# Optimization experiments

Hardware: AMD Instinct MI355X
Metric: run time of the kernel (lower is better)

## Reference

```python
import math
import jax, jax.numpy as jnp
import numpy as np

B, S, D = 2, 2048, 3584
H, KVH, HD = 28, 4, 128
ROPE_THETA = 1000000.0

def setup_inputs() -> dict:
    key = jax.random.key(0)
    k1, k2, k3, k4, k5 = jax.random.split(key, 5)
    s = 0.02
    return {
        'hidden_states': jax.random.normal(k1, (B, S, D), jnp.float32),
        'Wq': jax.random.normal(k2, (D, H * HD), jnp.float32) * s,
        'Wk': jax.random.normal(k3, (D, KVH * HD), jnp.float32) * s,
        'Wv': jax.random.normal(k4, (D, KVH * HD), jnp.float32) * s,
        'Wo': jax.random.normal(k5, (H * HD, D), jnp.float32) * s,
    }

def _rotate_half(x):
    x1, x2 = x[..., :x.shape[-1] // 2], x[..., x.shape[-1] // 2:]
    return jnp.concatenate((-x2, x1), axis=-1)

def _rope_tables(seq_len, dim, base):
    inv_freq = 1.0 / base ** (jnp.arange(0, dim, 2, dtype=jnp.float32) / dim)
    t = jnp.arange(seq_len, dtype=jnp.float32)
    freqs = jnp.outer(t, inv_freq)  # [S, dim/2]
    emb = jnp.concatenate((freqs, freqs), axis=-1)  # [S, dim]
    return jnp.cos(emb), jnp.sin(emb)

def reference(hidden_states, Wq, Wk, Wv, Wo):
    b, s, _ = hidden_states.shape
    q = (hidden_states @ Wq).reshape(b, s, H, HD)
    k = (hidden_states @ Wk).reshape(b, s, KVH, HD)
    v = (hidden_states @ Wv).reshape(b, s, KVH, HD)

    cos, sin = _rope_tables(s, HD, ROPE_THETA)
    cos = cos.astype(q.dtype)[None, :, None, :]  # [1,S,1,HD]
    sin = sin.astype(q.dtype)[None, :, None, :]
    q = q * cos + _rotate_half(q) * sin
    k = k * cos + _rotate_half(k) * sin

    groups = H // KVH  # 7
    k = jnp.repeat(k, groups, axis=2)
    v = jnp.repeat(v, groups, axis=2)

    q = jnp.transpose(q, (0, 2, 1, 3))  # [B,H,S,HD]
    k = jnp.transpose(k, (0, 2, 1, 3))
    v = jnp.transpose(v, (0, 2, 1, 3))

    scale = 1.0 / math.sqrt(HD)
    scores = jnp.einsum('bhqd,bhkd->bhqk', q, k) * scale
    causal = jnp.tril(jnp.ones((s, s), dtype=bool))[None, None]
    scores = scores + jnp.where(causal, 0.0, -1e9).astype(scores.dtype)
    attn = jax.nn.softmax(scores, axis=-1)
    out = jnp.einsum('bhqk,bhkd->bhqd', attn, v)
    out = jnp.transpose(out, (0, 2, 1, 3)).reshape(b, s, H * HD)
    return out @ Wo
```

## Files before the change

kernel.cpp:

```cpp
#include <hip/hip_runtime.h>
#include <hip/hip_bf16.h>
#include <cstdint>

typedef __attribute__((ext_vector_type(8))) __bf16 bf16x8;
typedef __attribute__((ext_vector_type(4))) float f32x4;
typedef unsigned short u16;

#define B_    2
#define S_    2048
#define D_    3584
#define H_    28
#define KVH_  4
#define HD_   128
#define GQA_  7
#define QKVN  4608
#define QK2SCALE 0.12751744416014806f

#define WAITV(N) asm volatile("s_waitcnt vmcnt(" #N ")" ::: "memory")
#define WAITL(N) asm volatile("s_waitcnt lgkmcnt(" #N ")" ::: "memory")

__device__ __forceinline__ u16 f2bf(float f){
  union { float f; uint32_t u; } v; v.f = f;
  uint32_t u = v.u + 0x7fffu + ((v.u >> 16) & 1u);
  return (u16)(u >> 16);
}
__device__ __forceinline__ float bf2f(u16 h){
  union { uint32_t u; float f; } v; v.u = ((uint32_t)h) << 16; return v.f;
}
__device__ __forceinline__ float exp2a(float x){
  float r; asm("v_exp_f32 %0, %1" : "=v"(r) : "v"(x)); return r;
}
__device__ __forceinline__ uint32_t cvtpk(float lo, float hi){
  uint32_t r; asm("v_cvt_pk_bf16_f32 %0, %1, %2" : "=v"(r) : "v"(lo), "v"(hi)); return r;
}

typedef void __attribute__((address_space(1))) as1void;
typedef void __attribute__((address_space(3))) as3void;
__device__ __forceinline__ void gload16(const void* g, void* l){
  __builtin_amdgcn_global_load_lds((as1void*)g, (as3void*)l, 16, 0, 0);
}

__global__ __launch_bounds__(256) void convx_kernel(const float* __restrict__ in, u16* __restrict__ outp, int n4){
  int i = blockIdx.x*256 + threadIdx.x;
  if (i < n4){
    float4 v = ((const float4*)in)[i];
    ushort4 o; o.x=f2bf(v.x); o.y=f2bf(v.y); o.z=f2bf(v.z); o.w=f2bf(v.w);
    ((ushort4*)outp)[i] = o;
  }
}

__global__ __launch_bounds__(256) void tconv_kernel(const float* __restrict__ in, u16* __restrict__ outp, int R, int C){
  __shared__ float t[32][33];
  int r = threadIdx.x >> 5, c = threadIdx.x & 31;
  int r0 = blockIdx.y*32, c0 = blockIdx.x*32;
  #pragma unroll
  for (int i=0;i<4;i++) t[r+8*i][c] = in[(size_t)(r0 + r + 8*i)*C + c0 + c];
  __syncthreads();
  #pragma unroll
  for (int i=0;i<4;i++) outp[(size_t)(c0 + r + 8*i)*R + r0 + c] = f2bf(t[c][r+8*i]);
}

__global__ __launch_bounds__(256) void tbf16_kernel(const u16* __restrict__ in, u16* __restrict__ outp, int R, int C, int instride){
  const u16* inb = in + (size_t)blockIdx.z*R*instride;
  u16* outb = outp + (size_t)blockIdx.z*R*C;
  __shared__ u16 t[32][33];
  int r = threadIdx.x >> 5, c = threadIdx.x & 31;
  int r0 = blockIdx.y*32, c0 = blockIdx.x*32;
  #pragma unroll
  for (int i=0;i<4;i++) t[r+8*i][c] = inb[(size_t)(r0+r+8*i)*instride + c0+c];
  __syncthreads();
  #pragma unroll
  for (int i=0;i<4;i++) outb[(size_t)(c0+r+8*i)*R + r0+c] = t[c][r+8*i];
}

__global__ __launch_bounds__(256) void ropetab_kernel(float* __restrict__ cost, float* __restrict__ sint){
  int i = blockIdx.x*256 + threadIdx.x;
  int s = i >> 6, d = i & 63;
  float inv = powf(1.0e6f, -(float)d * (1.0f/64.0f));
  float a = (float)s * inv;
  cost[i] = cosf(a); sint[i] = sinf(a);
}

__global__ __launch_bounds__(256) void rope_kernel(u16* __restrict__ x, const float* __restrict__ cost,
                                                   const float* __restrict__ sint){
  int i = blockIdx.x*256 + threadIdx.x;
  int d = i & 63;
  int h = (i >> 6) & 31;
  int bs = i >> 11;
  int s = bs & (S_-1);
  float sc = (h < H_) ? QK2SCALE : 1.0f;
  size_t base = (size_t)bs*QKVN + (size_t)h*128 + d;
  float x0 = bf2f(x[base]), x1 = bf2f(x[base+64]);
  float cv = cost[s*64+d], sv = sint[s*64+d];
  x[base]    = f2bf((x0*cv - x1*sv)*sc);
  x[base+64] = f2bf((x1*cv + x0*sv)*sc);
}

__global__ __launch_bounds__(256) void gemm128_kernel(const u16* __restrict__ A, const u16* __restrict__ Bt,
                                                      u16* __restrict__ C, int M, int N, int K, int ldc, int coloff){
  __shared__ u16 As[128*32];
  __shared__ u16 Bs[128*32];
  const int tid = threadIdx.x;
  const int l = tid & 63, lg = l >> 4, lm = l & 15;
  const int w = tid >> 6, wr = w >> 1, wc = w & 1;
  const int m0 = blockIdx.y * 128, n0 = blockIdx.x * 128;

  f32x4 acc[4][4];
  #pragma unroll
  for (int m=0;m<4;++m)
    #pragma unroll
    for (int n=0;n<4;++n) acc[m][n] = (f32x4){0.f,0.f,0.f,0.f};

  const int nkt = K >> 5;
  for (int kt = 0; kt < nkt; ++kt){
    __syncthreads();
    const int kb = kt*32;
    #pragma unroll
    for (int j = 0; j < 2; ++j){
      int g = j*256 + tid;
      int row = g >> 2, wi = g & 3;
      int ksrc = kb + ((wi ^ (row & 3)) << 3);
      gload16(A  + (size_t)(m0+row)*K + ksrc, (char*)As + j*4096 + (tid & 192)*16);
      gload16(Bt + (size_t)(n0+row)*K + ksrc, (char*)Bs + j*4096 + (tid & 192)*16);
    }
    __syncthreads();
    bf16x8 af[4], bfr[4];
    #pragma unroll
    for (int m = 0; m < 4; ++m){
      int r = wr*64 + m*16 + lm;
      af[m] = *(const bf16x8*)((const char*)As + r*64 + (lg ^ (r & 3))*16);
    }
    #pragma unroll
    for (int n = 0; n < 4; ++n){
      int r = wc*64 + n*16 + lm;
      bfr[n] = *(const bf16x8*)((const char*)Bs + r*64 + (lg ^ (r & 3))*16);
    }
    #pragma unroll
    for (int m = 0; m < 4; ++m)
      #pragma unroll
      for (int n = 0; n < 4; ++n)
        acc[m][n] = __builtin_amdgcn_mfma_f32_16x16x32_bf16(af[m], bfr[n], acc[m][n], 0,0,0);
  }
  #pragma unroll
  for (int m=0;m<4;++m)
    #pragma unroll
    for (int n=0;n<4;++n)
      #pragma unroll
      for (int r=0;r<4;++r){
        int row = m0 + wr*64 + m*16 + lg*4 + r;
        int col = coloff + n0 + wc*64 + n*16 + lm;
        C[(size_t)row*ldc + col] = f2bf(acc[m][n][r]);
      }
}

template<bool OUTF32>
__global__ __launch_bounds__(512) void gemm256_kernel(const u16* __restrict__ A, const u16* __restrict__ Bt,
                                                      void* __restrict__ Cv, int M, int N, int K, int nbx,
                                                      int ldc, int coloff){
  extern __shared__ char lds[];
  const int tid = threadIdx.x;
  const int l = tid & 63, lg = l >> 4, lm = l & 15;
  const int w = tid >> 6, wr = w >> 2, wc = w & 3;
  const int srow = tid >> 3, swi = tid & 7;

  const int nwg = (int)gridDim.x;
  const int q8 = nwg >> 3, r8 = nwg & 7;
  const int xcd = blockIdx.x & 7, pos = blockIdx.x >> 3;
  const int wg = (xcd < r8 ? xcd*(q8+1) : r8*(q8+1) + (xcd - r8)*q8) + pos;
  const int m0 = (wg / nbx) * 256, n0 = (wg % nbx) * 256;

  f32x4 acc[8][4];
  #pragma unroll
  for (int m=0;m<8;++m)
    #pragma unroll
    for (int n=0;n<4;++n) acc[m][n] = (f32x4){0.f,0.f,0.f,0.f};
  bf16x8 aF[8][2], bF[4][2];

  auto stage = [&](int T, int ht){
    const u16* p = (ht < 2) ? (A + (size_t)(m0 + (ht << 7))*K)
                            : (Bt + (size_t)(n0 + ((ht - 2) << 7))*K);
    char* d = lds + ((size_t)(T & 1) << 16) + (ht << 14) + ((tid & 448) << 4);
    #pragma unroll
    for (int j = 0; j < 2; ++j){
      int r = (j << 6) + srow;
      gload16(p + (size_t)r*K + (size_t)T*64 + ((swi ^ (r & 7)) << 3), d + (j << 13));
    }
  };
  auto ldA = [&](int c, int mh){
    const char* base = lds + (c << 16) + (wr << 14);
    #pragma unroll
    for (int m = 0; m < 4; ++m){
      int r = ((mh*4 + m) << 4) + lm;
      #pragma unroll
      for (int kk = 0; kk < 2; ++kk)
        aF[mh*4+m][kk] = *(const bf16x8*)(base + r*128 + (((kk*4 + lg) ^ (r & 7)) << 4));
    }
  };
  auto ldB = [&](int c, int nh){
    #pragma unroll
    for (int n = 0; n < 2; ++n){
      int rb = wc*64 + ((nh*2 + n) << 4) + lm;
      const char* base = lds + (c << 16) + 32768 + ((rb >> 7) << 14);
      int ri = rb & 127;
      #pragma unroll
      for (int kk = 0; kk < 2; ++kk)
        bF[nh*2+n][kk] = *(const bf16x8*)(base + ri*128 + (((kk*4 + lg) ^ (ri & 7)) << 4));
    }
  };
  auto mmaQ = [&](int mh, int nh){
    __builtin_amdgcn_s_setprio(1);
    #pragma unroll
    for (int m = 0; m < 4; ++m)
      #pragma unroll
      for (int n = 0; n < 2; ++n)
        #pragma unroll
        for (int kk = 0; kk < 2; ++kk)
          acc[mh*4+m][nh*2+n] = __builtin_amdgcn_mfma_f32_16x16x32_bf16(
              aF[mh*4+m][kk], bF[nh*2+n][kk], acc[mh*4+m][nh*2+n], 0,0,0);
    __builtin_amdgcn_s_setprio(0);
  };

  const int nkt = K >> 6;
  stage(0,0); stage(0,1); stage(0,2); stage(0,3);
  stage(1,2); stage(1,0); stage(1,1);
  WAITV(6);
  __builtin_amdgcn_s_barrier();

  for (int t = 0; t < nkt; ++t){
    const int c = t & 1;
    ldA(c,0); ldB(c,0); ldB(c,1);
    if (t + 1 < nkt) stage(t+1, 3);
    WAITL(4);
    __builtin_amdgcn_s_barrier();
    mmaQ(0,0);
    WAITL(0);
    __builtin_amdgcn_s_barrier();
    ldA(c,1);
    if (t + 2 < nkt) stage(t+2, 2);
    __builtin_amdgcn_s_barrier();
    mmaQ(0,1);
    WAITL(0);
    __builtin_amdgcn_s_barrier();
    if (t + 2 < nkt) stage(t+2, 0);
    __builtin_amdgcn_s_barrier();
    mmaQ(1,0);
    __builtin_amdgcn_s_barrier();
    if (t + 2 < nkt){ stage(t+2, 1); WAITV(6); }
    else if (t + 1 < nkt){ WAITV(0); }
    __builtin_amdgcn_s_barrier();
    mmaQ(1,1);
    __builtin_amdgcn_s_barrier();
  }

  #pragma unroll
  for (int m = 0; m < 8; ++m)
    #pragma unroll
    for (int n = 0; n < 4; ++n)
      #pragma unroll
      for (int r = 0; r < 4; ++r){
        int row = m0 + wr*128 + m*16 + lg*4 + r;
        int col = coloff + n0 + wc*64 + n*16 + lm;
        if (OUTF32) ((float*)Cv)[(size_t)row*ldc + col] = acc[m][n][r];
        else        ((u16*)Cv)[(size_t)row*ldc + col] = f2bf(acc[m][n][r]);
      }
}

__global__ __launch_bounds__(512, 4) void attn_kernel(const u16* __restrict__ QKV, const u16* __restrict__ Vt,
                                                      u16* __restrict__ O){
  __shared__ u16 Kl[2][8192];
  __shared__ u16 Vl[8192];
  const int id = blockIdx.x;
  const int qt = (S_/128 - 1) - id/(H_*B_);
  const int hb = id % (H_*B_);
  const int h = hb % H_, b = hb / H_;
  const int kvh = h / GQA_;
  const int tid = threadIdx.x;
  const int w = tid >> 6, l = tid & 63, lg = l >> 4, lm = l & 15;

  const int qrowA = qt*128 + w*16 + lm;
  const u16* qptr = QKV + (size_t)(b*S_ + qrowA)*QKVN + h*HD_;
  bf16x8 qf[4];
  #pragma unroll
  for (int ks = 0; ks < 4; ++ks) qf[ks] = *(const bf16x8*)(qptr + ks*32 + lg*8);
  WAITV(0);
  asm volatile("" :: "v"(qf[0]), "v"(qf[1]), "v"(qf[2]), "v"(qf[3]));

  const int qcol  = qrowA;
  const int qrowD = qt*128 + w*16 + lg*4;
  float m_run = -3.0e38f, l_run = 0.0f;
  f32x4 oacc[8];
  #pragma unroll
  for (int dn=0;dn<8;++dn) oacc[dn] = (f32x4){0.f,0.f,0.f,0.f};

  const u16* Kbase = QKV + (size_t)(b*S_)*QKVN + H_*HD_ + kvh*HD_;
  const u16* Vbase = Vt + (size_t)(b*KVH_ + kvh)*HD_*S_;

  auto stageK = [&](int bufi, int ktv){
    const int kb = ktv*64;
    #pragma unroll
    for (int j = 0; j < 2; ++j){
      int g = j*512 + tid;
      int kp = g >> 4, wik = g & 15;
      gload16(Kbase + (size_t)(kb + kp)*QKVN + (wik ^ (kp & 7))*8,
              (char*)Kl + bufi*16384 + j*8192 + (tid & 448)*16);
    }
  };
  auto stageV = [&](int ktv){
    const int kb = ktv*64;
    #pragma unroll
    for (int j = 0; j < 2; ++j){
      int g = j*512 + tid;
      int dd = g >> 3, wiv = g & 7;
      gload16(Vbase + (size_t)dd*S_ + kb + (wiv ^ (dd & 7))*8,
              (char*)Vl + j*8192 + (tid & 448)*16);
    }
  };

  const int nkt = 2*qt + 2;
  int cur = 0;
  stageK(0, 0); stageV(0); stageK(1, 1);

  auto iter = [&](int kt, bool domask){
    if (kt + 1 < nkt){ WAITV(2); }
    else             { WAITV(0); }
    __builtin_amdgcn_s_barrier();
    const int cb = cur*16384;

    f32x4 sf[4];
    __builtin_amdgcn_s_setprio(1);
    #pragma unroll
    for (int n = 0; n < 4; ++n){
      sf[n] = (f32x4){0.f,0.f,0.f,0.f};
      int kp = n*16 + lm;
      #pragma unroll
      for (int ks = 0; ks < 4; ++ks){
        bf16x8 kf = *(const bf16x8*)((const char*)Kl + cb + kp*256 + (((ks*4 + lg) ^ (kp & 7))*16));
        sf[n] = __builtin_amdgcn_mfma_f32_16x16x32_bf16(kf, qf[ks], sf[n], 0,0,0);
      }
    }
    __builtin_amdgcn_s_setprio(0);

    float p[4][4];
    float rmax = -3.0e38f;
    #pragma unroll
    for (int n=0;n<4;++n)
      #pragma unroll
      for (int r=0;r<4;++r){
        float v = sf[n][r];
        if (domask && (kt*64 + n*16 + lg*4 + r) > qcol) v -= 1.0e9f;
        p[n][r] = v;
        rmax = fmaxf(rmax, v);
      }
    rmax = fmaxf(rmax, __shfl_xor(rmax, 16, 64));
    rmax = fmaxf(rmax, __shfl_xor(rmax, 32, 64));

    if (__any(rmax > m_run + 8.0f)){
      float mn = fmaxf(m_run, rmax);
      float corr = exp2a(m_run - mn);
      m_run = mn;
      l_run *= corr;
      float corr_r[4];
      #pragma unroll
      for (int r=0;r<4;++r) corr_r[r] = __shfl(corr, lg*4 + r, 64);
      #pragma unroll
      for (int dn=0;dn<8;++dn)
        #pragma unroll
        for (int r=0;r<4;++r) oacc[dn][r] *= corr_r[r];
    }
    float psum = 0.f;
    #pragma unroll
    for (int n=0;n<4;++n)
      #pragma unroll
      for (int r=0;r<4;++r){ p[n][r] = exp2a(p[n][r] - m_run); psum += p[n][r]; }
    l_run += psum;

    __builtin_amdgcn_s_barrier();
    char* Pl = (char*)Kl + cb;
    {
      int q_ = w*16 + lm;
      #pragma unroll
      for (int n=0;n<4;++n)
        #pragma unroll
        for (int j=0;j<2;++j){
          uint32_t pk = cvtpk(p[n][2*j], p[n][2*j+1]);
          int kp = n*16 + lg*4 + 2*j;
          *(uint32_t*)(Pl + q_*128 + (((kp >> 3) ^ (q_ & 7))*16) + (kp & 7)*2) = pk;
        }
    }

    __builtin_amdgcn_s_setprio(1);
    #pragma unroll
    for (int ks=0; ks<2; ++ks){
      int q_ = w*16 + lm;
      bf16x8 pf = *(const bf16x8*)(Pl + q_*128 + (((ks*4 + lg) ^ (q_ & 7))*16));
      #pragma unroll
      for (int dn=0;dn<8;++dn){
        int dd = dn*16 + lm;
        bf16x8 vf = *(const bf16x8*)((const char*)Vl + dd*128 + (((ks*4 + lg) ^ (dd & 7))*16));
        oacc[dn] = __builtin_amdgcn_mfma_f32_16x16x32_bf16(pf, vf, oacc[dn], 0,0,0);
      }
    }
    __builtin_amdgcn_s_setprio(0);

    WAITL(0);
    __builtin_amdgcn_s_barrier();
    if (kt + 1 < nkt) stageV(kt+1);
    if (kt + 2 < nkt) stageK(cur, kt+2);
    cur ^= 1;
  };

  for (int kt = 0; kt < nkt - 2; ++kt) iter(kt, false);
  iter(nkt-2, true);
  iter(nkt-1, true);

  l_run += __shfl_xor(l_run, 16, 64);
  l_run += __shfl_xor(l_run, 32, 64);
  float inv = 1.0f / l_run;
  float inv_r[4];
  #pragma unroll
  for (int r=0;r<4;++r) inv_r[r] = __shfl(inv, lg*4 + r, 64);
  #pragma unroll
  for (int dn=0;dn<8;++dn)
    #pragma unroll
    for (int r=0;r<4;++r)
      O[(size_t)(b*S_ + qrowD + r)*(H_*HD_) + h*HD_ + dn*16 + lm] = f2bf(oacc[dn][r]*inv_r[r]);
}

extern "C" void kernel_launch(void* const* d_in, const int* in_sizes, int n_in,
                              void* d_out, int out_size, void* d_ws, size_t ws_size,
                              hipStream_t stream) {
  const float* X  = (const float*)d_in[0];
  const float* Wq = (const float*)d_in[1];
  const float* Wk = (const float*)d_in[2];
  const float* Wv = (const float*)d_in[3];
  const float* Wo = (const float*)d_in[4];
  float* out = (float*)d_out;

  char* ws = (char*)d_ws;
  size_t off = 0;
  auto alloc = [&](size_t bytes)->void*{ void* p = ws + off; off += (bytes + 255) & ~(size_t)255; return p; };
  const size_t MB = (size_t)B_*S_;
  u16* Xb   = (u16*)alloc(MB*D_*2);
  u16* Wqkv = (u16*)alloc((size_t)D_*QKVN*2);
  u16* Wot  = (u16*)alloc((size_t)H_*HD_*D_*2);
  u16* QKVb = (u16*)alloc(MB*QKVN*2);
  float* cost = (float*)alloc((size_t)S_*64*4);
  float* sint = (float*)alloc((size_t)S_*64*4);
  u16* AO  = Xb;
  u16* Vtg = Wqkv;

  (void)hipFuncSetAttribute(reinterpret_cast<const void*>(gemm256_kernel<false>),
                            hipFuncAttributeMaxDynamicSharedMemorySize, 131072);
  (void)hipFuncSetAttribute(reinterpret_cast<const void*>(gemm256_kernel<true>),
                            hipFuncAttributeMaxDynamicSharedMemorySize, 131072);

  convx_kernel<<<dim3((MB*D_/4 + 255)/256), 256, 0, stream>>>(X, Xb, (int)(MB*D_/4));
  tconv_kernel<<<dim3(D_/32, D_/32), 256, 0, stream>>>(Wq, Wqkv, D_, H_*HD_);
  tconv_kernel<<<dim3((KVH_*HD_)/32, D_/32), 256, 0, stream>>>(Wk, Wqkv + (size_t)(H_*HD_)*D_, D_, KVH_*HD_);
  tconv_kernel<<<dim3((KVH_*HD_)/32, D_/32), 256, 0, stream>>>(Wv, Wqkv + (size_t)(H_*HD_ + KVH_*HD_)*D_, D_, KVH_*HD_);
  tconv_kernel<<<dim3(D_/32, (H_*HD_)/32), 256, 0, stream>>>(Wo, Wot, H_*HD_, D_);
  ropetab_kernel<<<dim3(S_*64/256), 256, 0, stream>>>(cost, sint);
  gemm256_kernel<false><<<dim3((D_/256)*(MB/256)), 512, 131072, stream>>>(Xb, Wqkv, QKVb, (int)MB, D_, D_, D_/256, QKVN, 0);
  gemm128_kernel<<<dim3((KVH_*HD_*2)/128, MB/128), 256, 0, stream>>>(Xb, Wqkv + (size_t)(H_*HD_)*D_, QKVb, (int)MB, KVH_*HD_*2, D_, QKVN, H_*HD_);
  rope_kernel<<<dim3(MB*32*64/256), 256, 0, stream>>>(QKVb, cost, sint);
  tbf16_kernel<<<dim3((KVH_*HD_)/32, S_/32, B_), 256, 0, stream>>>(QKVb + (H_+KVH_)*HD_, Vtg, S_, KVH_*HD_, QKVN);
  attn_kernel<<<dim3((S_/128)*H_*B_), 512, 0, stream>>>(QKVb, Vtg, AO);
  gemm256_kernel<true><<<dim3((D_/256)*(MB/256)), 512, 131072, stream>>>(AO, Wot, out, (int)MB, D_, H_*HD_, D_/256, D_, 0);
}
```

Baseline: 447.0 us.

## Shrink large GEMM tile to 256x128 with simple double-buffered K=32 pipeline

```diff
diff --git a/kernel.cpp b/kernel.cpp
--- a/kernel.cpp
+++ b/kernel.cpp
@@ -154,111 +154,80 @@
 }
 
 template<bool OUTF32>
-__global__ __launch_bounds__(512) void gemm256_kernel(const u16* __restrict__ A, const u16* __restrict__ Bt,
-                                                      void* __restrict__ Cv, int M, int N, int K, int nbx,
-                                                      int ldc, int coloff){
-  extern __shared__ char lds[];
+__global__ __launch_bounds__(512, 4) void gemm256_kernel(const u16* __restrict__ A, const u16* __restrict__ Bt,
+                                                         void* __restrict__ Cv, int M, int N, int K, int nbx,
+                                                         int ldc, int coloff){
+  __shared__ char lds[49152];
   const int tid = threadIdx.x;
   const int l = tid & 63, lg = l >> 4, lm = l & 15;
-  const int w = tid >> 6, wr = w >> 2, wc = w & 3;
-  const int srow = tid >> 3, swi = tid & 7;
+  const int w = tid >> 6, wr = w >> 1, wc = w & 1;
 
   const int nwg = (int)gridDim.x;
   const int q8 = nwg >> 3, r8 = nwg & 7;
   const int xcd = blockIdx.x & 7, pos = blockIdx.x >> 3;
   const int wg = (xcd < r8 ? xcd*(q8+1) : r8*(q8+1) + (xcd - r8)*q8) + pos;
-  const int m0 = (wg / nbx) * 256, n0 = (wg % nbx) * 256;
-
-  f32x4 acc[8][4];
-  #pragma unroll
-  for (int m=0;m<8;++m)
+  const int m0 = (wg / nbx) * 256, n0 = (wg % nbx) * 128;
+
+  f32x4 acc[4][4];
+  #pragma unroll
+  for (int m=0;m<4;++m)
     #pragma unroll
     for (int n=0;n<4;++n) acc[m][n] = (f32x4){0.f,0.f,0.f,0.f};
-  bf16x8 aF[8][2], bF[4][2];
-
-  auto stage = [&](int T, int ht){
-    const u16* p = (ht < 2) ? (A + (size_t)(m0 + (ht << 7))*K)
-                            : (Bt + (size_t)(n0 + ((ht - 2) << 7))*K);
-    char* d = lds + ((size_t)(T & 1) << 16) + (ht << 14) + ((tid & 448) << 4);
+
+  auto stage = [&](int T){
+    const int kb = (T & 0x3fffffff)*32;
+    char* base = lds + (size_t)(T & 1)*24576;
     #pragma unroll
     for (int j = 0; j < 2; ++j){
-      int r = (j << 6) + srow;
-      gload16(p + (size_t)r*K + (size_t)T*64 + ((swi ^ (r & 7)) << 3), d + (j << 13));
-    }
+      int g = j*512 + tid;
+      int row = g >> 2, wi = g & 3;
+      gload16(A + (size_t)(m0+row)*K + kb + ((wi ^ (row & 3)) << 3),
+              base + j*8192 + (tid & 448)*16);
+    }
+    { int row = tid >> 2, wi = tid & 3;
+      gload16(Bt + (size_t)(n0+row)*K + kb + ((wi ^ (row & 3)) << 3),
+              base + 16384 + (tid & 448)*16); }
   };
-  auto ldA = [&](int c, int mh){
-    const char* base = lds + (c << 16) + (wr << 14);
+
+  const int nkt = K >> 5;
+  stage(0); stage(1);
+  int cur = 0;
+  for (int t = 0; t < nkt; ++t){
+    if (t + 1 < nkt){ WAITV(3); }
+    else            { WAITV(0); }
+    __builtin_amdgcn_s_barrier();
+    const char* base = lds + (size_t)cur*24576;
+    bf16x8 aF[4], bF[4];
     #pragma unroll
     for (int m = 0; m < 4; ++m){
-      int r = ((mh*4 + m) << 4) + lm;
-      #pragma unroll
-      for (int kk = 0; kk < 2; ++kk)
-        aF[mh*4+m][kk] = *(const bf16x8*)(base + r*128 + (((kk*4 + lg) ^ (r & 7)) << 4));
-    }
-  };
-  auto ldB = [&](int c, int nh){
-    #pragma unroll
-    for (int n = 0; n < 2; ++n){
-      int rb = wc*64 + ((nh*2 + n) << 4) + lm;
-      const char* base = lds + (c << 16) + 32768 + ((rb >> 7) << 14);
-      int ri = rb & 127;
-      #pragma unroll
-      for (int kk = 0; kk < 2; ++kk)
-        bF[nh*2+n][kk] = *(const bf16x8*)(base + ri*128 + (((kk*4 + lg) ^ (ri & 7)) << 4));
-    }
-  };
-  auto mmaQ = [&](int mh, int nh){
+      int r = wr*64 + m*16 + lm;
+      aF[m] = *(const bf16x8*)(base + r*64 + ((lg ^ (r & 3)) << 4));
+    }
+    #pragma unroll
+    for (int n = 0; n < 4; ++n){
+      int r = wc*64 + n*16 + lm;
+      bF[n] = *(const bf16x8*)(base + 16384 + r*64 + ((lg ^ (r & 3)) << 4));
+    }
     __builtin_amdgcn_s_setprio(1);
     #pragma unroll
     for (int m = 0; m < 4; ++m)
       #pragma unroll
-      for (int n = 0; n < 2; ++n)
-        #pragma unroll
-        for (int kk = 0; kk < 2; ++kk)
-          acc[mh*4+m][nh*2+n] = __builtin_amdgcn_mfma_f32_16x16x32_bf16(
-              aF[mh*4+m][kk], bF[nh*2+n][kk], acc[mh*4+m][nh*2+n], 0,0,0);
+      for (int n = 0; n < 4; ++n)
+        acc[m][n] = __builtin_amdgcn_mfma_f32_16x16x32_bf16(aF[m], bF[n], acc[m][n], 0,0,0);
     __builtin_amdgcn_s_setprio(0);
-  };
-
-  const int nkt = K >> 6;
-  stage(0,0); stage(0,1); stage(0,2); stage(0,3);
-  stage(1,2); stage(1,0); stage(1,1);
-  WAITV(6);
-  __builtin_amdgcn_s_barrier();
-
-  for (int t = 0; t < nkt; ++t){
-    const int c = t & 1;
-    ldA(c,0); ldB(c,0); ldB(c,1);
-    if (t + 1 < nkt) stage(t+1, 3);
-    WAITL(4);
-    __builtin_amdgcn_s_barrier();
-    mmaQ(0,0);
     WAITL(0);
     __builtin_amdgcn_s_barrier();
-    ldA(c,1);
-    if (t + 2 < nkt) stage(t+2, 2);
-    __builtin_amdgcn_s_barrier();
-    mmaQ(0,1);
-    WAITL(0);
-    __builtin_amdgcn_s_barrier();
-    if (t + 2 < nkt) stage(t+2, 0);
-    __builtin_amdgcn_s_barrier();
-    mmaQ(1,0);
-    __builtin_amdgcn_s_barrier();
-    if (t + 2 < nkt){ stage(t+2, 1); WAITV(6); }
-    else if (t + 1 < nkt){ WAITV(0); }
-    __builtin_amdgcn_s_barrier();
-    mmaQ(1,1);
-    __builtin_amdgcn_s_barrier();
+    if (t + 2 < nkt) stage(t+2);
+    cur ^= 1;
   }
 
   #pragma unroll
-  for (int m = 0; m < 8; ++m)
+  for (int m = 0; m < 4; ++m)
     #pragma unroll
     for (int n = 0; n < 4; ++n)
       #pragma unroll
       for (int r = 0; r < 4; ++r){
-        int row = m0 + wr*128 + m*16 + lg*4 + r;
+        int row = m0 + wr*64 + m*16 + lg*4 + r;
         int col = coloff + n0 + wc*64 + n*16 + lm;
         if (OUTF32) ((float*)Cv)[(size_t)row*ldc + col] = acc[m][n][r];
         else        ((u16*)Cv)[(size_t)row*ldc + col] = f2bf(acc[m][n][r]);
@@ -449,21 +418,16 @@
   u16* AO  = Xb;
   u16* Vtg = Wqkv;
 
-  (void)hipFuncSetAttribute(reinterpret_cast<const void*>(gemm256_kernel<false>),
-                            hipFuncAttributeMaxDynamicSharedMemorySize, 131072);
-  (void)hipFuncSetAttribute(reinterpret_cast<const void*>(gemm256_kernel<true>),
-                            hipFuncAttributeMaxDynamicSharedMemorySize, 131072);
-
   convx_kernel<<<dim3((MB*D_/4 + 255)/256), 256, 0, stream>>>(X, Xb, (int)(MB*D_/4));
   tconv_kernel<<<dim3(D_/32, D_/32), 256, 0, stream>>>(Wq, Wqkv, D_, H_*HD_);
   tconv_kernel<<<dim3((KVH_*HD_)/32, D_/32), 256, 0, stream>>>(Wk, Wqkv + (size_t)(H_*HD_)*D_, D_, KVH_*HD_);
   tconv_kernel<<<dim3((KVH_*HD_)/32, D_/32), 256, 0, stream>>>(Wv, Wqkv + (size_t)(H_*HD_ + KVH_*HD_)*D_, D_, KVH_*HD_);
   tconv_kernel<<<dim3(D_/32, (H_*HD_)/32), 256, 0, stream>>>(Wo, Wot, H_*HD_, D_);
   ropetab_kernel<<<dim3(S_*64/256), 256, 0, stream>>>(cost, sint);
-  gemm256_kernel<false><<<dim3((D_/256)*(MB/256)), 512, 131072, stream>>>(Xb, Wqkv, QKVb, (int)MB, D_, D_, D_/256, QKVN, 0);
+  gemm256_kernel<false><<<dim3((MB/256)*(D_/128)), 512, 0, stream>>>(Xb, Wqkv, QKVb, (int)MB, D_, D_, D_/128, QKVN, 0);
   gemm128_kernel<<<dim3((KVH_*HD_*2)/128, MB/128), 256, 0, stream>>>(Xb, Wqkv + (size_t)(H_*HD_)*D_, QKVb, (int)MB, KVH_*HD_*2, D_, QKVN, H_*HD_);
   rope_kernel<<<dim3(MB*32*64/256), 256, 0, stream>>>(QKVb, cost, sint);
   tbf16_kernel<<<dim3((KVH_*HD_)/32, S_/32, B_), 256, 0, stream>>>(QKVb + (H_+KVH_)*HD_, Vtg, S_, KVH_*HD_, QKVN);
   attn_kernel<<<dim3((S_/128)*H_*B_), 512, 0, stream>>>(QKVb, Vtg, AO);
-  gemm256_kernel<true><<<dim3((D_/256)*(MB/256)), 512, 131072, stream>>>(AO, Wot, out, (int)MB, D_, H_*HD_, D_/256, D_, 0);
-}
+  gemm256_kernel<true><<<dim3((MB/256)*(D_/128)), 512, 0, stream>>>(AO, Wot, out, (int)MB, D_, H_*HD_, D_/128, D_, 0);
+}
```

Result: slower. 468.8 us (+4.9%).

## Fuse RoPE into QKV GEMM epilogues by remapping output column ownership

Applied to the files above, without the earlier changes.

```diff
diff --git a/kernel.cpp b/kernel.cpp
--- a/kernel.cpp
+++ b/kernel.cpp
@@ -81,23 +81,10 @@
   cost[i] = cosf(a); sint[i] = sinf(a);
 }
 
-__global__ __launch_bounds__(256) void rope_kernel(u16* __restrict__ x, const float* __restrict__ cost,
-                                                   const float* __restrict__ sint){
-  int i = blockIdx.x*256 + threadIdx.x;
-  int d = i & 63;
-  int h = (i >> 6) & 31;
-  int bs = i >> 11;
-  int s = bs & (S_-1);
-  float sc = (h < H_) ? QK2SCALE : 1.0f;
-  size_t base = (size_t)bs*QKVN + (size_t)h*128 + d;
-  float x0 = bf2f(x[base]), x1 = bf2f(x[base+64]);
-  float cv = cost[s*64+d], sv = sint[s*64+d];
-  x[base]    = f2bf((x0*cv - x1*sv)*sc);
-  x[base+64] = f2bf((x1*cv + x0*sv)*sc);
-}
-
 __global__ __launch_bounds__(256) void gemm128_kernel(const u16* __restrict__ A, const u16* __restrict__ Bt,
-                                                      u16* __restrict__ C, int M, int N, int K, int ldc, int coloff){
+                                                      u16* __restrict__ C, int M, int N, int K, int ldc, int coloff,
+                                                      const float* __restrict__ cost, const float* __restrict__ sint,
+                                                      int ropeNmax){
   __shared__ u16 As[128*32];
   __shared__ u16 Bs[128*32];
   const int tid = threadIdx.x;
@@ -132,7 +119,7 @@
     }
     #pragma unroll
     for (int n = 0; n < 4; ++n){
-      int r = wc*64 + n*16 + lm;
+      int r = (wc<<5) + ((n>>1)<<6) + ((n&1)<<4) + lm;
       bfr[n] = *(const bf16x8*)((const char*)Bs + r*64 + (lg ^ (r & 3))*16);
     }
     #pragma unroll
@@ -141,6 +128,24 @@
       for (int n = 0; n < 4; ++n)
         acc[m][n] = __builtin_amdgcn_mfma_f32_16x16x32_bf16(af[m], bfr[n], acc[m][n], 0,0,0);
   }
+
+  if (n0 < ropeNmax){
+    #pragma unroll
+    for (int m=0;m<4;++m)
+      #pragma unroll
+      for (int n=0;n<2;++n)
+        #pragma unroll
+        for (int r=0;r<4;++r){
+          int row = m0 + wr*64 + m*16 + lg*4 + r;
+          int s = row & (S_-1);
+          int d = (wc<<5) + (n<<4) + lm;
+          float cv = cost[s*64+d], sv = sint[s*64+d];
+          float lo = acc[m][n][r], hi = acc[m][n+2][r];
+          acc[m][n][r]   = lo*cv - hi*sv;
+          acc[m][n+2][r] = hi*cv + lo*sv;
+        }
+  }
+
   #pragma unroll
   for (int m=0;m<4;++m)
     #pragma unroll
@@ -148,15 +153,16 @@
       #pragma unroll
       for (int r=0;r<4;++r){
         int row = m0 + wr*64 + m*16 + lg*4 + r;
-        int col = coloff + n0 + wc*64 + n*16 + lm;
+        int col = coloff + n0 + (wc<<5) + ((n>>1)<<6) + ((n&1)<<4) + lm;
         C[(size_t)row*ldc + col] = f2bf(acc[m][n][r]);
       }
 }
 
-template<bool OUTF32>
+template<bool OUTF32, bool ROPEQ>
 __global__ __launch_bounds__(512) void gemm256_kernel(const u16* __restrict__ A, const u16* __restrict__ Bt,
                                                       void* __restrict__ Cv, int M, int N, int K, int nbx,
-                                                      int ldc, int coloff){
+                                                      int ldc, int coloff,
+                                                      const float* __restrict__ cost, const float* __restrict__ sint){
   extern __shared__ char lds[];
   const int tid = threadIdx.x;
   const int l = tid & 63, lg = l >> 4, lm = l & 15;
@@ -199,12 +205,13 @@
   auto ldB = [&](int c, int nh){
     #pragma unroll
     for (int n = 0; n < 2; ++n){
-      int rb = wc*64 + ((nh*2 + n) << 4) + lm;
+      int f = nh*2 + n;
+      int rb = ((wc>>1)<<7) + ((wc&1)<<5) + ((f>>1)<<6) + ((f&1)<<4) + lm;
       const char* base = lds + (c << 16) + 32768 + ((rb >> 7) << 14);
       int ri = rb & 127;
       #pragma unroll
       for (int kk = 0; kk < 2; ++kk)
-        bF[nh*2+n][kk] = *(const bf16x8*)(base + ri*128 + (((kk*4 + lg) ^ (ri & 7)) << 4));
+        bF[f][kk] = *(const bf16x8*)(base + ri*128 + (((kk*4 + lg) ^ (ri & 7)) << 4));
     }
   };
   auto mmaQ = [&](int mh, int nh){
@@ -252,6 +259,23 @@
     __builtin_amdgcn_s_barrier();
   }
 
+  if (ROPEQ){
+    #pragma unroll
+    for (int m=0;m<8;++m)
+      #pragma unroll
+      for (int n=0;n<2;++n)
+        #pragma unroll
+        for (int r=0;r<4;++r){
+          int row = m0 + wr*128 + m*16 + lg*4 + r;
+          int s = row & (S_-1);
+          int d = ((wc&1)<<5) + (n<<4) + lm;
+          float cv = cost[s*64+d], sv = sint[s*64+d];
+          float lo = acc[m][n][r], hi = acc[m][n+2][r];
+          acc[m][n][r]   = (lo*cv - hi*sv)*QK2SCALE;
+          acc[m][n+2][r] = (hi*cv + lo*sv)*QK2SCALE;
+        }
+  }
+
   #pragma unroll
   for (int m = 0; m < 8; ++m)
     #pragma unroll
@@ -259,7 +283,7 @@
       #pragma unroll
       for (int r = 0; r < 4; ++r){
         int row = m0 + wr*128 + m*16 + lg*4 + r;
-        int col = coloff + n0 + wc*64 + n*16 + lm;
+        int col = coloff + n0 + ((wc>>1)<<7) + ((wc&1)<<5) + ((n>>1)<<6) + ((n&1)<<4) + lm;
         if (OUTF32) ((float*)Cv)[(size_t)row*ldc + col] = acc[m][n][r];
         else        ((u16*)Cv)[(size_t)row*ldc + col] = f2bf(acc[m][n][r]);
       }
@@ -449,9 +473,9 @@
   u16* AO  = Xb;
   u16* Vtg = Wqkv;
 
-  (void)hipFuncSetAttribute(reinterpret_cast<const void*>(gemm256_kernel<false>),
+  (void)hipFuncSetAttribute(reinterpret_cast<const void*>(gemm256_kernel<false, true>),
                             hipFuncAttributeMaxDynamicSharedMemorySize, 131072);
-  (void)hipFuncSetAttribute(reinterpret_cast<const void*>(gemm256_kernel<true>),
+  (void)hipFuncSetAttribute(reinterpret_cast<const void*>(gemm256_kernel<true, false>),
                             hipFuncAttributeMaxDynamicSharedMemorySize, 131072);
 
   convx_kernel<<<dim3((MB*D_/4 + 255)/256), 256, 0, stream>>>(X, Xb, (int)(MB*D_/4));
@@ -460,10 +484,12 @@
   tconv_kernel<<<dim3((KVH_*HD_)/32, D_/32), 256, 0, stream>>>(Wv, Wqkv + (size_t)(H_*HD_ + KVH_*HD_)*D_, D_, KVH_*HD_);
   tconv_kernel<<<dim3(D_/32, (H_*HD_)/32), 256, 0, stream>>>(Wo, Wot, H_*HD_, D_);
   ropetab_kernel<<<dim3(S_*64/256), 256, 0, stream>>>(cost, sint);
-  gemm256_kernel<false><<<dim3((D_/256)*(MB/256)), 512, 131072, stream>>>(Xb, Wqkv, QKVb, (int)MB, D_, D_, D_/256, QKVN, 0);
-  gemm128_kernel<<<dim3((KVH_*HD_*2)/128, MB/128), 256, 0, stream>>>(Xb, Wqkv + (size_t)(H_*HD_)*D_, QKVb, (int)MB, KVH_*HD_*2, D_, QKVN, H_*HD_);
-  rope_kernel<<<dim3(MB*32*64/256), 256, 0, stream>>>(QKVb, cost, sint);
+  gemm256_kernel<false, true><<<dim3((D_/256)*(MB/256)), 512, 131072, stream>>>(
+      Xb, Wqkv, QKVb, (int)MB, D_, D_, D_/256, QKVN, 0, cost, sint);
+  gemm128_kernel<<<dim3((KVH_*HD_*2)/128, MB/128), 256, 0, stream>>>(
+      Xb, Wqkv + (size_t)(H_*HD_)*D_, QKVb, (int)MB, KVH_*HD_*2, D_, QKVN, H_*HD_, cost, sint, KVH_*HD_);
   tbf16_kernel<<<dim3((KVH_*HD_)/32, S_/32, B_), 256, 0, stream>>>(QKVb + (H_+KVH_)*HD_, Vtg, S_, KVH_*HD_, QKVN);
   attn_kernel<<<dim3((S_/128)*H_*B_), 512, 0, stream>>>(QKVb, Vtg, AO);
-  gemm256_kernel<true><<<dim3((D_/256)*(MB/256)), 512, 131072, stream>>>(AO, Wot, out, (int)MB, D_, H_*HD_, D_/256, D_, 0);
-}
+  gemm256_kernel<true, false><<<dim3((D_/256)*(MB/256)), 512, 131072, stream>>>(
+      AO, Wot, out, (int)MB, D_, H_*HD_, D_/256, D_, 0, cost, sint);
+}
```

New measurement: 437.2 us. 1.02x faster.
